# Optimization experiments

Hardware: AMD Instinct MI355X
Metric: run time of the kernel (lower is better)

The kernel has to match this reference:

```python
import jax, jax.numpy as jnp
import numpy as np

EPS_RMS = 1e-6  # mmfreelm RMSNorm default eps

def _rmsnorm(x, w):
    var = jnp.mean(x * x, axis=-1, keepdims=True)
    return x * jax.lax.rsqrt(var + EPS_RMS) * w

def _activation_quant(x):
    # per-token absmax int8 quant (BitNet b1.58 activation quant)
    scale = 127.0 / jnp.clip(jnp.max(jnp.abs(x), axis=-1, keepdims=True), 1e-5)
    return jnp.clip(jnp.round(x * scale), -128.0, 127.0) / scale

def _weight_quant(w):
    # ternary quant with global mean-abs scale
    scale = 1.0 / jnp.clip(jnp.mean(jnp.abs(w)), 1e-5)
    return jnp.clip(jnp.round(w * scale), -1.0, 1.0) / scale

def _nm_mask(w, n, m):
    # keep top-n by |w| in every group of m along the input (last) dim
    O, I = w.shape
    g = jnp.abs(w).reshape(-1, m)            # [G, m]
    _, idx = jax.lax.top_k(g, n)             # [G, n]
    rows = jnp.arange(g.shape[0])[:, None]
    mask = jnp.zeros_like(g).at[rows, idx].set(1.0)
    return mask.reshape(O, I)

def setup_inputs() -> dict:
    key = jax.random.key(0)
    k1, k2 = jax.random.split(key)
    B, S, IN, OUT = 4, 2048, 4096, 11008
    x = jax.random.normal(k1, (B, S, IN), dtype=jnp.float32)
    weight = jax.random.normal(k2, (OUT, IN), dtype=jnp.float32) * 0.02
    norm_weight = jnp.ones((IN,), dtype=jnp.float32)
    return {"x": x, "weight": weight, "norm_weight": norm_weight,
            "sparse_n": 2, "sparse_m": 4}

def reference(x, weight, norm_weight, sparse_n, sparse_m):
    x_norm = _rmsnorm(x, norm_weight)
    # STE quantization (forward value == quantized value)
    x_q = x_norm + jax.lax.stop_gradient(_activation_quant(x_norm) - x_norm)
    w_q = weight + jax.lax.stop_gradient(_weight_quant(weight) - weight)
    mask = jax.lax.stop_gradient(_nm_mask(w_q, sparse_n, sparse_m))
    w_sparse = w_q * mask                    # [OUT, IN]
    return jnp.einsum('bsi,oi->bso', x_q, w_sparse)
```

## Files before the change

### kernel.cpp

```cpp
#include <hip/hip_runtime.h>
#include <stdint.h>

#define IN_DIM 4096
#define OUT_DIM 11008
#define TOKENS 8192
#define WN (45088768L)
#define NKT128 32

typedef int int4v __attribute__((ext_vector_type(4)));
#define AS1 __attribute__((address_space(1)))
#define AS3 __attribute__((address_space(3)))

__device__ __forceinline__ float bf2f(uint32_t u16) {
  union { uint32_t i; float f; } v; v.i = u16 << 16; return v.f;
}
__device__ __forceinline__ bool probe_bf16(const void* nw) {
  return ((const uint16_t*)nw)[0] == 0x3F80u;
}

__global__ __launch_bounds__(256) void k_wabs(const void* __restrict__ wv,
                                              const void* __restrict__ nwv,
                                              double* __restrict__ partial) {
  const bool b16 = probe_bf16(nwv);
  const long tid = (long)blockIdx.x * 256 + threadIdx.x;
  const long stride = (long)gridDim.x * 256;
  double s = 0.0;
  if (b16) {
    const uint4* w = (const uint4*)wv;
    for (long i = tid; i < WN / 8; i += stride) {
      uint4 v = w[i];
      uint32_t a[4] = {v.x, v.y, v.z, v.w};
      float t = 0.f;
#pragma unroll
      for (int j = 0; j < 4; j++)
        t += fabsf(bf2f(a[j] & 0xffffu)) + fabsf(bf2f(a[j] >> 16));
      s += (double)t;
    }
  } else {
    const float4* w = (const float4*)wv;
    for (long i = tid; i < WN / 4; i += stride) {
      float4 v = w[i];
      s += (double)(fabsf(v.x) + fabsf(v.y) + fabsf(v.z) + fabsf(v.w));
    }
  }
#pragma unroll
  for (int off = 32; off > 0; off >>= 1) s += __shfl_down(s, off);
  __shared__ double sd[4];
  if ((threadIdx.x & 63) == 0) sd[threadIdx.x >> 6] = s;
  __syncthreads();
  if (threadIdx.x == 0) partial[blockIdx.x] = (sd[0] + sd[1]) + (sd[2] + sd[3]);
}

__global__ __launch_bounds__(256) void k_wscale(const double* __restrict__ partial,
                                                float* __restrict__ hdr) {
  double s = 0.0;
  for (int i = threadIdx.x; i < 2048; i += 256) s += partial[i];
#pragma unroll
  for (int off = 32; off > 0; off >>= 1) s += __shfl_down(s, off);
  __shared__ double sd[4];
  if ((threadIdx.x & 63) == 0) sd[threadIdx.x >> 6] = s;
  __syncthreads();
  if (threadIdx.x == 0) {
    double mean = ((sd[0] + sd[1]) + (sd[2] + sd[3])) / (double)WN;
    float meanc = (float)mean;
    if (meanc < 1e-5f) meanc = 1e-5f;
    float wscale = 1.0f / meanc;
    hdr[0] = wscale;
    hdr[1] = 1.0f / wscale;
  }
}

__global__ __launch_bounds__(256) void k_act(const void* __restrict__ xv,
                                             const void* __restrict__ nwv,
                                             int8_t* __restrict__ qx,
                                             float* __restrict__ invsx) {
  const bool b16 = probe_bf16(nwv);
  const int t = blockIdx.x;
  const int tx = threadIdx.x;
  float xw[16];
  float ss = 0.f, mx = 0.f;
  if (b16) {
    const uint16_t* xr = (const uint16_t*)xv + (long)t * IN_DIM;
    const uint16_t* nw = (const uint16_t*)nwv;
#pragma unroll
    for (int c = 0; c < 2; c++) {
      uint4 vx = ((const uint4*)xr)[tx * 2 + c];
      uint4 vn = ((const uint4*)nw)[tx * 2 + c];
      uint32_t ax[4] = {vx.x, vx.y, vx.z, vx.w};
      uint32_t an[4] = {vn.x, vn.y, vn.z, vn.w};
#pragma unroll
      for (int j = 0; j < 4; j++) {
        float x0 = bf2f(ax[j] & 0xffffu), x1 = bf2f(ax[j] >> 16);
        float n0 = bf2f(an[j] & 0xffffu), n1 = bf2f(an[j] >> 16);
        ss += x0 * x0 + x1 * x1;
        float p0 = x0 * n0, p1 = x1 * n1;
        xw[c * 8 + j * 2]     = p0;
        xw[c * 8 + j * 2 + 1] = p1;
        mx = fmaxf(mx, fmaxf(fabsf(p0), fabsf(p1)));
      }
    }
  } else {
    const float* xr = (const float*)xv + (long)t * IN_DIM;
    const float* nw = (const float*)nwv;
#pragma unroll
    for (int c = 0; c < 4; c++) {
      float4 vx = ((const float4*)xr)[tx * 4 + c];
      float4 vn = ((const float4*)nw)[tx * 4 + c];
      ss += vx.x * vx.x + vx.y * vx.y + vx.z * vx.z + vx.w * vx.w;
      float p0 = vx.x * vn.x, p1 = vx.y * vn.y, p2 = vx.z * vn.z, p3 = vx.w * vn.w;
      xw[c * 4 + 0] = p0; xw[c * 4 + 1] = p1; xw[c * 4 + 2] = p2; xw[c * 4 + 3] = p3;
      mx = fmaxf(mx, fmaxf(fmaxf(fabsf(p0), fabsf(p1)), fmaxf(fabsf(p2), fabsf(p3))));
    }
  }
#pragma unroll
  for (int off = 32; off > 0; off >>= 1) {
    ss += __shfl_down(ss, off);
    mx = fmaxf(mx, __shfl_down(mx, off));
  }
  __shared__ float s_ss[4], s_mx[4];
  __shared__ float bc[1];
  if ((tx & 63) == 0) { s_ss[tx >> 6] = ss; s_mx[tx >> 6] = mx; }
  __syncthreads();
  if (tx == 0) {
    float sst = (s_ss[0] + s_ss[1]) + (s_ss[2] + s_ss[3]);
    float mxt = fmaxf(fmaxf(s_mx[0], s_mx[1]), fmaxf(s_mx[2], s_mx[3]));
    float var = sst / (float)IN_DIM;
    float rms = 1.0f / sqrtf(var + 1e-6f);
    float amax = rms * mxt;
    if (amax < 1e-5f) amax = 1e-5f;
    float scale = 127.0f / amax;
    bc[0] = rms * scale;
    invsx[t] = 1.0f / scale;
  }
  __syncthreads();
  float rsc = bc[0];
  uint32_t pw[4];
#pragma unroll
  for (int d = 0; d < 4; d++) {
    uint32_t v = 0;
#pragma unroll
    for (int j = 0; j < 4; j++) {
      float q = rintf(xw[d * 4 + j] * rsc);
      q = fminf(fmaxf(q, -128.f), 127.f);
      int qi = (int)q;
      v |= ((uint32_t)(qi & 0xff)) << (8 * j);
    }
    pw[d] = v;
  }
  uint4 st; st.x = pw[0]; st.y = pw[1]; st.z = pw[2]; st.w = pw[3];
  ((uint4*)(qx + (long)t * IN_DIM))[tx] = st;
}

__global__ __launch_bounds__(256) void k_wq(const void* __restrict__ wv,
                                            const void* __restrict__ nwv,
                                            const float* __restrict__ hdr,
                                            int8_t* __restrict__ qw) {
  const bool b16 = probe_bf16(nwv);
  const long i = (long)blockIdx.x * 256 + threadIdx.x;
  const float wscale = hdr[0];
  float f[8];
  if (b16) {
    uint4 v = ((const uint4*)wv)[i];
    uint32_t a[4] = {v.x, v.y, v.z, v.w};
#pragma unroll
    for (int j = 0; j < 4; j++) {
      f[j * 2]     = bf2f(a[j] & 0xffffu);
      f[j * 2 + 1] = bf2f(a[j] >> 16);
    }
  } else {
    float4 v0 = ((const float4*)wv)[i * 2];
    float4 v1 = ((const float4*)wv)[i * 2 + 1];
    f[0] = v0.x; f[1] = v0.y; f[2] = v0.z; f[3] = v0.w;
    f[4] = v1.x; f[5] = v1.y; f[6] = v1.z; f[7] = v1.w;
  }
  int q[8];
#pragma unroll
  for (int j = 0; j < 8; j++) {
    float qf = rintf(f[j] * wscale);
    qf = fminf(fmaxf(qf, -1.f), 1.f);
    q[j] = (int)qf;
  }
#pragma unroll
  for (int g = 0; g < 2; g++) {
    int cnt = 0;
#pragma unroll
    for (int j = 0; j < 4; j++) {
      int idx = g * 4 + j;
      if (q[idx] != 0) { cnt++; if (cnt > 2) q[idx] = 0; }
    }
  }
  uint32_t lo = 0, hi = 0;
#pragma unroll
  for (int j = 0; j < 4; j++) lo |= ((uint32_t)(q[j] & 0xff)) << (8 * j);
#pragma unroll
  for (int j = 0; j < 4; j++) hi |= ((uint32_t)(q[4 + j] & 0xff)) << (8 * j);
  uint2 st; st.x = lo; st.y = hi;
  ((uint2*)qw)[i] = st;
}

__global__ __launch_bounds__(512, 2) void k_gemm(const int8_t* __restrict__ qx,
                                                 const int8_t* __restrict__ qw,
                                                 const float* __restrict__ invsx,
                                                 const float* __restrict__ hdr,
                                                 float* __restrict__ out) {
  __shared__ __align__(16) int8_t sA[2][256 * 128];
  __shared__ __align__(16) int8_t sB[2][256 * 128];

  const int tx = threadIdx.x;
  const int wave = tx >> 6, lane = tx & 63;
  const int wr = wave >> 2, wc = wave & 3;
  const int fr = lane & 15;
  const int fg = lane >> 4;

  const int bid = blockIdx.x;
  const int swz = (bid & 7) * 172 + (bid >> 3);
  const int m0 = (swz & 31) * 256;
  const int n0 = (swz >> 5) * 256;

  const int srow = tx >> 3;
  const int scol = ((tx & 7) ^ ((tx >> 4) & 7)) * 16;
  const int8_t* gA = qx + (long)(m0 + srow) * IN_DIM + scol;
  const int8_t* gB = qw + (long)(n0 + srow) * IN_DIM + scol;
  int8_t* const sA0 = &sA[0][0];
  int8_t* const sB0 = &sB[0][0];

  auto stageA = [&](int t, int half) {
    if (t >= NKT128) return;
    int8_t* base = sA0 + (t & 1) * (256 * 128);
#pragma unroll
    for (int l = 0; l < 2; ++l) {
      const int rb = half * 128 + l * 64;
      __builtin_amdgcn_global_load_lds(
          (const AS1 void*)(gA + (long)t * 128 + (long)rb * IN_DIM),
          (AS3 void*)(base + rb * 128 + wave * 1024), 16, 0, 0);
    }
  };
  auto stageB = [&](int t, int half) {
    if (t >= NKT128) return;
    int8_t* base = sB0 + (t & 1) * (256 * 128);
#pragma unroll
    for (int l = 0; l < 2; ++l) {
      const int rb = half * 128 + l * 64;
      __builtin_amdgcn_global_load_lds(
          (const AS1 void*)(gB + (long)t * 128 + (long)rb * IN_DIM),
          (AS3 void*)(base + rb * 128 + wave * 1024), 16, 0, 0);
    }
  };

  int offA[8][2], offB[4][2];
#pragma unroll
  for (int mi = 0; mi < 8; ++mi) {
    const int row = wr * 128 + mi * 16 + fr;
    const int xr = (row >> 1) & 7;
#pragma unroll
    for (int ks = 0; ks < 2; ++ks)
      offA[mi][ks] = row * 128 + (((ks * 4 + fg) ^ xr) * 16);
  }
#pragma unroll
  for (int ni = 0; ni < 4; ++ni) {
    const int row = wc * 64 + ni * 16 + fr;
    const int xr = (row >> 1) & 7;
#pragma unroll
    for (int ks = 0; ks < 2; ++ks)
      offB[ni][ks] = row * 128 + (((ks * 4 + fg) ^ xr) * 16);
  }

  int4v acc[8][4];
#pragma unroll
  for (int mi = 0; mi < 8; ++mi)
#pragma unroll
    for (int ni = 0; ni < 4; ++ni) {
      acc[mi][ni][0] = 0; acc[mi][ni][1] = 0; acc[mi][ni][2] = 0; acc[mi][ni][3] = 0;
    }

  stageA(0, 0); stageA(0, 1); stageB(0, 0); stageB(0, 1);
  stageA(1, 0); stageA(1, 1);
  asm volatile("s_waitcnt vmcnt(4)" ::: "memory");
  __builtin_amdgcn_s_barrier();

  int4v a[8][2];
  int4v bf[2][2];

#pragma unroll 2
  for (int t = 0; t < NKT128; ++t) {
    const int bofs = (t & 1) * (256 * 128);

#pragma unroll
    for (int j = 0; j < 2; ++j) {
      bf[j][0] = *(const int4v*)(sB0 + bofs + offB[j][0]);
      bf[j][1] = *(const int4v*)(sB0 + bofs + offB[j][1]);
    }
#pragma unroll
    for (int mi = 0; mi < 4; ++mi) {
      a[mi][0] = *(const int4v*)(sA0 + bofs + offA[mi][0]);
      a[mi][1] = *(const int4v*)(sA0 + bofs + offA[mi][1]);
    }
    stageB(t + 1, 0);
    asm volatile("s_waitcnt lgkmcnt(8)" ::: "memory");
    __builtin_amdgcn_s_barrier();
    asm volatile("s_waitcnt lgkmcnt(0)" ::: "memory");
    __builtin_amdgcn_s_setprio(1);
#pragma unroll
    for (int mi = 0; mi < 4; ++mi)
#pragma unroll
      for (int j = 0; j < 2; ++j)
#pragma unroll
        for (int ks = 0; ks < 2; ++ks)
          acc[mi][j] = __builtin_amdgcn_mfma_i32_16x16x64_i8(a[mi][ks], bf[j][ks], acc[mi][j], 0, 0, 0);
    __builtin_amdgcn_s_setprio(0);
    __builtin_amdgcn_s_barrier();

#pragma unroll
    for (int mi = 4; mi < 8; ++mi) {
      a[mi][0] = *(const int4v*)(sA0 + bofs + offA[mi][0]);
      a[mi][1] = *(const int4v*)(sA0 + bofs + offA[mi][1]);
    }
    stageB(t + 1, 1);
    __builtin_amdgcn_s_barrier();
    asm volatile("s_waitcnt lgkmcnt(0)" ::: "memory");
    __builtin_amdgcn_s_setprio(1);
#pragma unroll
    for (int mi = 4; mi < 8; ++mi)
#pragma unroll
      for (int j = 0; j < 2; ++j)
#pragma unroll
        for (int ks = 0; ks < 2; ++ks)
          acc[mi][j] = __builtin_amdgcn_mfma_i32_16x16x64_i8(a[mi][ks], bf[j][ks], acc[mi][j], 0, 0, 0);
    __builtin_amdgcn_s_setprio(0);
    __builtin_amdgcn_s_barrier();

#pragma unroll
    for (int j = 0; j < 2; ++j) {
      bf[j][0] = *(const int4v*)(sB0 + bofs + offB[2 + j][0]);
      bf[j][1] = *(const int4v*)(sB0 + bofs + offB[2 + j][1]);
    }
    stageA(t + 2, 0);
    __builtin_amdgcn_s_barrier();
    asm volatile("s_waitcnt lgkmcnt(0)" ::: "memory");
    __builtin_amdgcn_s_setprio(1);
#pragma unroll
    for (int mi = 0; mi < 4; ++mi)
#pragma unroll
      for (int j = 0; j < 2; ++j)
#pragma unroll
        for (int ks = 0; ks < 2; ++ks)
          acc[mi][2 + j] = __builtin_amdgcn_mfma_i32_16x16x64_i8(a[mi][ks], bf[j][ks], acc[mi][2 + j], 0, 0, 0);
    __builtin_amdgcn_s_setprio(0);
    __builtin_amdgcn_s_barrier();

    stageA(t + 2, 1);
    if (t < NKT128 - 2) {
      asm volatile("s_waitcnt vmcnt(4)" ::: "memory");
    } else {
      asm volatile("s_waitcnt vmcnt(0)" ::: "memory");
    }
    __builtin_amdgcn_s_barrier();
    __builtin_amdgcn_s_setprio(1);
#pragma unroll
    for (int mi = 4; mi < 8; ++mi)
#pragma unroll
      for (int j = 0; j < 2; ++j)
#pragma unroll
        for (int ks = 0; ks < 2; ++ks)
          acc[mi][2 + j] = __builtin_amdgcn_mfma_i32_16x16x64_i8(a[mi][ks], bf[j][ks], acc[mi][2 + j], 0, 0, 0);
    __builtin_amdgcn_s_setprio(0);
    __builtin_amdgcn_s_barrier();
  }

  const float winv = hdr[1];
#pragma unroll
  for (int mi = 0; mi < 8; ++mi) {
    const int rbase = m0 + wr * 128 + mi * 16 + (lane >> 4) * 4;
#pragma unroll
    for (int r = 0; r < 4; ++r) {
      const int trow = rbase + r;
      const float fs = invsx[trow] * winv;
      const long ob = (long)trow * OUT_DIM + n0 + wc * 64 + fr;
#pragma unroll
      for (int ni = 0; ni < 4; ++ni) {
        out[ob + ni * 16] = (float)acc[mi][ni][r] * fs;
      }
    }
  }
}

extern "C" void kernel_launch(void* const* d_in, const int* in_sizes, int n_in,
                              void* d_out, int out_size, void* d_ws, size_t ws_size,
                              hipStream_t stream) {
  const void* x  = d_in[0];
  const void* w  = d_in[1];
  const void* nw = d_in[2];
  float* out = (float*)d_out;

  char* ws = (char*)d_ws;
  float*  hdr     = (float*)ws;
  double* partial = (double*)(ws + 1024);
  float*  invsx   = (float*)(ws + 20480);
  int8_t* qx      = (int8_t*)(ws + (1L << 20));
  int8_t* qw      = (int8_t*)(ws + 36L * (1L << 20));

  hipLaunchKernelGGL(k_wabs,   dim3(2048),   dim3(256), 0, stream, w, nw, partial);
  hipLaunchKernelGGL(k_wscale, dim3(1),      dim3(256), 0, stream, partial, hdr);
  hipLaunchKernelGGL(k_act,    dim3(TOKENS), dim3(256), 0, stream, x, nw, qx, invsx);
  hipLaunchKernelGGL(k_wq,     dim3(22016),  dim3(256), 0, stream, w, nw, hdr, qw);
  hipLaunchKernelGGL(k_gemm,   dim3(32 * 43), dim3(512), 0, stream,
                     qx, qw, invsx, hdr, out);
}
```

Measured before the change: 611.8 us.

## Simplify int8 GEMM main loop to a single-barrier double-buffered schedule

Replaces the hand-interleaved main loop with a plain double-buffered loop. The old loop used four quarter-phases, separate A/B staging with a two-tile A prefetch, explicit waitcnts and many barriers. The new loop issues the A and B global-to-LDS copies for the next tile, loads all LDS fragments at once, runs all MFMAs, and ends with one __syncthreads. The aim is to cut barrier and waitcnt overhead and give the compiler freedom to schedule. The cost is shallower prefetch and less overlap between LDS reads and MFMA work, plus higher register pressure from holding all A/B fragments at once.

```diff
diff --git a/kernel.cpp b/kernel.cpp
--- a/kernel.cpp
+++ b/kernel.cpp
@@ -224,26 +224,19 @@
   int8_t* const sA0 = &sA[0][0];
   int8_t* const sB0 = &sB[0][0];
 
-  auto stageA = [&](int t, int half) {
+  auto STAGE = [&](int t) {
     if (t >= NKT128) return;
-    int8_t* base = sA0 + (t & 1) * (256 * 128);
-#pragma unroll
-    for (int l = 0; l < 2; ++l) {
-      const int rb = half * 128 + l * 64;
+    int8_t* bA = sA0 + (t & 1) * (256 * 128);
+    int8_t* bB = sB0 + (t & 1) * (256 * 128);
+    const long ko = (long)t * 128;
+#pragma unroll
+    for (int rb = 0; rb < 256; rb += 64) {
       __builtin_amdgcn_global_load_lds(
-          (const AS1 void*)(gA + (long)t * 128 + (long)rb * IN_DIM),
-          (AS3 void*)(base + rb * 128 + wave * 1024), 16, 0, 0);
-    }
-  };
-  auto stageB = [&](int t, int half) {
-    if (t >= NKT128) return;
-    int8_t* base = sB0 + (t & 1) * (256 * 128);
-#pragma unroll
-    for (int l = 0; l < 2; ++l) {
-      const int rb = half * 128 + l * 64;
+          (const AS1 void*)(gA + ko + (long)rb * IN_DIM),
+          (AS3 void*)(bA + rb * 128 + wave * 1024), 16, 0, 0);
       __builtin_amdgcn_global_load_lds(
-          (const AS1 void*)(gB + (long)t * 128 + (long)rb * IN_DIM),
-          (AS3 void*)(base + rb * 128 + wave * 1024), 16, 0, 0);
+          (const AS1 void*)(gB + ko + (long)rb * IN_DIM),
+          (AS3 void*)(bB + rb * 128 + wave * 1024), 16, 0, 0);
     }
   };
 
@@ -273,98 +266,37 @@
       acc[mi][ni][0] = 0; acc[mi][ni][1] = 0; acc[mi][ni][2] = 0; acc[mi][ni][3] = 0;
     }
 
-  stageA(0, 0); stageA(0, 1); stageB(0, 0); stageB(0, 1);
-  stageA(1, 0); stageA(1, 1);
-  asm volatile("s_waitcnt vmcnt(4)" ::: "memory");
-  __builtin_amdgcn_s_barrier();
-
-  int4v a[8][2];
-  int4v bf[2][2];
-
-#pragma unroll 2
+  STAGE(0);
+  __syncthreads();
+
   for (int t = 0; t < NKT128; ++t) {
     const int bofs = (t & 1) * (256 * 128);
 
-#pragma unroll
-    for (int j = 0; j < 2; ++j) {
-      bf[j][0] = *(const int4v*)(sB0 + bofs + offB[j][0]);
-      bf[j][1] = *(const int4v*)(sB0 + bofs + offB[j][1]);
-    }
-#pragma unroll
-    for (int mi = 0; mi < 4; ++mi) {
+    STAGE(t + 1);
+
+    int4v a[8][2], b[4][2];
+#pragma unroll
+    for (int ni = 0; ni < 4; ++ni) {
+      b[ni][0] = *(const int4v*)(sB0 + bofs + offB[ni][0]);
+      b[ni][1] = *(const int4v*)(sB0 + bofs + offB[ni][1]);
+    }
+#pragma unroll
+    for (int mi = 0; mi < 8; ++mi) {
       a[mi][0] = *(const int4v*)(sA0 + bofs + offA[mi][0]);
       a[mi][1] = *(const int4v*)(sA0 + bofs + offA[mi][1]);
     }
-    stageB(t + 1, 0);
-    asm volatile("s_waitcnt lgkmcnt(8)" ::: "memory");
-    __builtin_amdgcn_s_barrier();
-    asm volatile("s_waitcnt lgkmcnt(0)" ::: "memory");
+
     __builtin_amdgcn_s_setprio(1);
 #pragma unroll
-    for (int mi = 0; mi < 4; ++mi)
-#pragma unroll
-      for (int j = 0; j < 2; ++j)
+    for (int mi = 0; mi < 8; ++mi)
+#pragma unroll
+      for (int ni = 0; ni < 4; ++ni)
 #pragma unroll
         for (int ks = 0; ks < 2; ++ks)
-          acc[mi][j] = __builtin_amdgcn_mfma_i32_16x16x64_i8(a[mi][ks], bf[j][ks], acc[mi][j], 0, 0, 0);
+          acc[mi][ni] = __builtin_amdgcn_mfma_i32_16x16x64_i8(a[mi][ks], b[ni][ks], acc[mi][ni], 0, 0, 0);
     __builtin_amdgcn_s_setprio(0);
-    __builtin_amdgcn_s_barrier();
-
-#pragma unroll
-    for (int mi = 4; mi < 8; ++mi) {
-      a[mi][0] = *(const int4v*)(sA0 + bofs + offA[mi][0]);
-      a[mi][1] = *(const int4v*)(sA0 + bofs + offA[mi][1]);
-    }
-    stageB(t + 1, 1);
-    __builtin_amdgcn_s_barrier();
-    asm volatile("s_waitcnt lgkmcnt(0)" ::: "memory");
-    __builtin_amdgcn_s_setprio(1);
-#pragma unroll
-    for (int mi = 4; mi < 8; ++mi)
-#pragma unroll
-      for (int j = 0; j < 2; ++j)
-#pragma unroll
-        for (int ks = 0; ks < 2; ++ks)
-          acc[mi][j] = __builtin_amdgcn_mfma_i32_16x16x64_i8(a[mi][ks], bf[j][ks], acc[mi][j], 0, 0, 0);
-    __builtin_amdgcn_s_setprio(0);
-    __builtin_amdgcn_s_barrier();
-
-#pragma unroll
-    for (int j = 0; j < 2; ++j) {
-      bf[j][0] = *(const int4v*)(sB0 + bofs + offB[2 + j][0]);
-      bf[j][1] = *(const int4v*)(sB0 + bofs + offB[2 + j][1]);
-    }
-    stageA(t + 2, 0);
-    __builtin_amdgcn_s_barrier();
-    asm volatile("s_waitcnt lgkmcnt(0)" ::: "memory");
-    __builtin_amdgcn_s_setprio(1);
-#pragma unroll
-    for (int mi = 0; mi < 4; ++mi)
-#pragma unroll
-      for (int j = 0; j < 2; ++j)
-#pragma unroll
-        for (int ks = 0; ks < 2; ++ks)
-          acc[mi][2 + j] = __builtin_amdgcn_mfma_i32_16x16x64_i8(a[mi][ks], bf[j][ks], acc[mi][2 + j], 0, 0, 0);
-    __builtin_amdgcn_s_setprio(0);
-    __builtin_amdgcn_s_barrier();
-
-    stageA(t + 2, 1);
-    if (t < NKT128 - 2) {
-      asm volatile("s_waitcnt vmcnt(4)" ::: "memory");
-    } else {
-      asm volatile("s_waitcnt vmcnt(0)" ::: "memory");
-    }
-    __builtin_amdgcn_s_barrier();
-    __builtin_amdgcn_s_setprio(1);
-#pragma unroll
-    for (int mi = 4; mi < 8; ++mi)
-#pragma unroll
-      for (int j = 0; j < 2; ++j)
-#pragma unroll
-        for (int ks = 0; ks < 2; ++ks)
-          acc[mi][2 + j] = __builtin_amdgcn_mfma_i32_16x16x64_i8(a[mi][ks], bf[j][ks], acc[mi][2 + j], 0, 0, 0);
-    __builtin_amdgcn_s_setprio(0);
-    __builtin_amdgcn_s_barrier();
+
+    __syncthreads();
   }
 
   const float winv = hdr[1];
```

New measurement: 631.4 us. 3.2% more time.

## Simplify int8 GEMM pipeline to whole-tile double buffering with one prefetch

Applied to the files above, without the earlier changes.

Replaces the staggered, half-tile prefetch schedule with a plain double buffer. Previously A was prefetched two k-tiles ahead and B one ahead, split across the four MFMA phases. Now both A and B for tile t+1 are issued at the top of each iteration, followed by a full vmcnt(0) wait at the end. The manual lgkmcnt waits and the unroll-2 pragma are dropped, and the B fragments are split into separate register arrays. This cuts scheduling complexity and may reduce register pressure, but global-load latency now has only one iteration of MFMA work to hide behind. Each iteration also ends in a full memory drain.

```diff
diff --git a/kernel.cpp b/kernel.cpp
--- a/kernel.cpp
+++ b/kernel.cpp
@@ -224,26 +224,19 @@
   int8_t* const sA0 = &sA[0][0];
   int8_t* const sB0 = &sB[0][0];
 
-  auto stageA = [&](int t, int half) {
+  auto STAGE = [&](int t) {
     if (t >= NKT128) return;
-    int8_t* base = sA0 + (t & 1) * (256 * 128);
-#pragma unroll
-    for (int l = 0; l < 2; ++l) {
-      const int rb = half * 128 + l * 64;
+    int8_t* bA = sA0 + (t & 1) * 32768;
+    int8_t* bB = sB0 + (t & 1) * 32768;
+    const long ko = (long)t * 128;
+#pragma unroll
+    for (int rb = 0; rb < 256; rb += 64) {
       __builtin_amdgcn_global_load_lds(
-          (const AS1 void*)(gA + (long)t * 128 + (long)rb * IN_DIM),
-          (AS3 void*)(base + rb * 128 + wave * 1024), 16, 0, 0);
-    }
-  };
-  auto stageB = [&](int t, int half) {
-    if (t >= NKT128) return;
-    int8_t* base = sB0 + (t & 1) * (256 * 128);
-#pragma unroll
-    for (int l = 0; l < 2; ++l) {
-      const int rb = half * 128 + l * 64;
+          (const AS1 void*)(gA + ko + (long)rb * IN_DIM),
+          (AS3 void*)(bA + rb * 128 + wave * 1024), 16, 0, 0);
       __builtin_amdgcn_global_load_lds(
-          (const AS1 void*)(gB + (long)t * 128 + (long)rb * IN_DIM),
-          (AS3 void*)(base + rb * 128 + wave * 1024), 16, 0, 0);
+          (const AS1 void*)(gB + ko + (long)rb * IN_DIM),
+          (AS3 void*)(bB + rb * 128 + wave * 1024), 16, 0, 0);
     }
   };
 
@@ -273,32 +266,27 @@
       acc[mi][ni][0] = 0; acc[mi][ni][1] = 0; acc[mi][ni][2] = 0; acc[mi][ni][3] = 0;
     }
 
-  stageA(0, 0); stageA(0, 1); stageB(0, 0); stageB(0, 1);
-  stageA(1, 0); stageA(1, 1);
-  asm volatile("s_waitcnt vmcnt(4)" ::: "memory");
+  STAGE(0);
+  asm volatile("s_waitcnt vmcnt(0)" ::: "memory");
   __builtin_amdgcn_s_barrier();
 
-  int4v a[8][2];
-  int4v bf[2][2];
-
-#pragma unroll 2
   for (int t = 0; t < NKT128; ++t) {
-    const int bofs = (t & 1) * (256 * 128);
-
+    const int bofs = (t & 1) * 32768;
+
+    STAGE(t + 1);
+
+    int4v a[8][2], b01[2][2];
 #pragma unroll
     for (int j = 0; j < 2; ++j) {
-      bf[j][0] = *(const int4v*)(sB0 + bofs + offB[j][0]);
-      bf[j][1] = *(const int4v*)(sB0 + bofs + offB[j][1]);
+      b01[j][0] = *(const int4v*)(sB0 + bofs + offB[j][0]);
+      b01[j][1] = *(const int4v*)(sB0 + bofs + offB[j][1]);
     }
 #pragma unroll
     for (int mi = 0; mi < 4; ++mi) {
       a[mi][0] = *(const int4v*)(sA0 + bofs + offA[mi][0]);
       a[mi][1] = *(const int4v*)(sA0 + bofs + offA[mi][1]);
     }
-    stageB(t + 1, 0);
-    asm volatile("s_waitcnt lgkmcnt(8)" ::: "memory");
-    __builtin_amdgcn_s_barrier();
-    asm volatile("s_waitcnt lgkmcnt(0)" ::: "memory");
+    __builtin_amdgcn_s_barrier();
     __builtin_amdgcn_s_setprio(1);
 #pragma unroll
     for (int mi = 0; mi < 4; ++mi)
@@ -306,7 +294,7 @@
       for (int j = 0; j < 2; ++j)
 #pragma unroll
         for (int ks = 0; ks < 2; ++ks)
-          acc[mi][j] = __builtin_amdgcn_mfma_i32_16x16x64_i8(a[mi][ks], bf[j][ks], acc[mi][j], 0, 0, 0);
+          acc[mi][j] = __builtin_amdgcn_mfma_i32_16x16x64_i8(a[mi][ks], b01[j][ks], acc[mi][j], 0, 0, 0);
     __builtin_amdgcn_s_setprio(0);
     __builtin_amdgcn_s_barrier();
 
@@ -315,9 +303,7 @@
       a[mi][0] = *(const int4v*)(sA0 + bofs + offA[mi][0]);
       a[mi][1] = *(const int4v*)(sA0 + bofs + offA[mi][1]);
     }
-    stageB(t + 1, 1);
-    __builtin_amdgcn_s_barrier();
-    asm volatile("s_waitcnt lgkmcnt(0)" ::: "memory");
+    __builtin_amdgcn_s_barrier();
     __builtin_amdgcn_s_setprio(1);
 #pragma unroll
     for (int mi = 4; mi < 8; ++mi)
@@ -325,18 +311,17 @@
       for (int j = 0; j < 2; ++j)
 #pragma unroll
         for (int ks = 0; ks < 2; ++ks)
-          acc[mi][j] = __builtin_amdgcn_mfma_i32_16x16x64_i8(a[mi][ks], bf[j][ks], acc[mi][j], 0, 0, 0);
+          acc[mi][j] = __builtin_amdgcn_mfma_i32_16x16x64_i8(a[mi][ks], b01[j][ks], acc[mi][j], 0, 0, 0);
     __builtin_amdgcn_s_setprio(0);
     __builtin_amdgcn_s_barrier();
 
+    int4v b23[2][2];
 #pragma unroll
     for (int j = 0; j < 2; ++j) {
-      bf[j][0] = *(const int4v*)(sB0 + bofs + offB[2 + j][0]);
-      bf[j][1] = *(const int4v*)(sB0 + bofs + offB[2 + j][1]);
-    }
-    stageA(t + 2, 0);
-    __builtin_amdgcn_s_barrier();
-    asm volatile("s_waitcnt lgkmcnt(0)" ::: "memory");
+      b23[j][0] = *(const int4v*)(sB0 + bofs + offB[2 + j][0]);
+      b23[j][1] = *(const int4v*)(sB0 + bofs + offB[2 + j][1]);
+    }
+    __builtin_amdgcn_s_barrier();
     __builtin_amdgcn_s_setprio(1);
 #pragma unroll
     for (int mi = 0; mi < 4; ++mi)
@@ -344,17 +329,10 @@
       for (int j = 0; j < 2; ++j)
 #pragma unroll
         for (int ks = 0; ks < 2; ++ks)
-          acc[mi][2 + j] = __builtin_amdgcn_mfma_i32_16x16x64_i8(a[mi][ks], bf[j][ks], acc[mi][2 + j], 0, 0, 0);
+          acc[mi][2 + j] = __builtin_amdgcn_mfma_i32_16x16x64_i8(a[mi][ks], b23[j][ks], acc[mi][2 + j], 0, 0, 0);
     __builtin_amdgcn_s_setprio(0);
     __builtin_amdgcn_s_barrier();
 
-    stageA(t + 2, 1);
-    if (t < NKT128 - 2) {
-      asm volatile("s_waitcnt vmcnt(4)" ::: "memory");
-    } else {
-      asm volatile("s_waitcnt vmcnt(0)" ::: "memory");
-    }
-    __builtin_amdgcn_s_barrier();
     __builtin_amdgcn_s_setprio(1);
 #pragma unroll
     for (int mi = 4; mi < 8; ++mi)
@@ -362,8 +340,9 @@
       for (int j = 0; j < 2; ++j)
 #pragma unroll
         for (int ks = 0; ks < 2; ++ks)
-          acc[mi][2 + j] = __builtin_amdgcn_mfma_i32_16x16x64_i8(a[mi][ks], bf[j][ks], acc[mi][2 + j], 0, 0, 0);
+          acc[mi][2 + j] = __builtin_amdgcn_mfma_i32_16x16x64_i8(a[mi][ks], b23[j][ks], acc[mi][2 + j], 0, 0, 0);
     __builtin_amdgcn_s_setprio(0);
+    asm volatile("s_waitcnt vmcnt(0)" ::: "memory");
     __builtin_amdgcn_s_barrier();
   }
 
```

New measurement: 692.7 us. +13.2%, slower.
